# Optimization experiments

Hardware: AMD Instinct MI355X
Metric: run time of the kernel (lower is better)

## Reference

```python
import jax, jax.numpy as jnp
from jax import lax
import numpy as np

EPS = 1e-5
BONES = [(0,1),(0,2),(1,3),(2,4),(5,7),(7,9),(6,8),(8,10),(11,13),(13,15),(12,14),(14,16)]


def _build_adj(num_joints=17):
    adj = np.eye(num_joints, dtype=np.float32)
    for i, j in BONES:
        adj[i, j] = 1.0
        adj[j, i] = 1.0
    d = adj.sum(1) ** -0.5
    return jnp.asarray(d[:, None] * adj * d[None, :])


def _bn(x, gamma, beta, axes):
    # training-mode BatchNorm: biased variance over `axes`
    mean = x.mean(axes, keepdims=True)
    var = ((x - mean) ** 2).mean(axes, keepdims=True)
    return (x - mean) * lax.rsqrt(var + EPS) * gamma + beta


def _gcn_block(x, adj, w, b, gamma, beta):
    # x: [N, V, Cin]; adjacency mixing then 1x1 conv (pointwise linear)
    x = jnp.einsum('nvc,vw->nwc', x, adj)
    x = jnp.einsum('nvc,oc->nvo', x, w) + b            # Conv1d(k=1): [N, V, Cout]
    x = _bn(x, gamma, beta, axes=(0, 1))               # BN over channel Cout
    return jax.nn.relu(x)


def setup_inputs() -> dict:
    key = jax.random.key(0)
    ks = jax.random.split(key, 16)
    B, T, V, C, H = 64, 512, 17, 2, 128
    s = 0.1
    return {
        'x':   jax.random.normal(ks[0], (B, T, V, C), jnp.float32),
        'adj': _build_adj(V),
        'w1':  jax.random.normal(ks[1], (64, C), jnp.float32) * s,
        'b1':  jax.random.normal(ks[2], (64,), jnp.float32) * s,
        'g1':  1.0 + jax.random.normal(ks[3], (64,), jnp.float32) * s,
        'be1': jax.random.normal(ks[4], (64,), jnp.float32) * s,
        'w2':  jax.random.normal(ks[5], (H, 64), jnp.float32) * s,
        'b2':  jax.random.normal(ks[6], (H,), jnp.float32) * s,
        'g2':  1.0 + jax.random.normal(ks[7], (H,), jnp.float32) * s,
        'be2': jax.random.normal(ks[8], (H,), jnp.float32) * s,
        'wt':  jax.random.normal(ks[9], (H, H * V, 3), jnp.float32) * 0.02,
        'bt':  jax.random.normal(ks[10], (H,), jnp.float32) * s,
        'gt':  1.0 + jax.random.normal(ks[11], (H,), jnp.float32) * s,
        'bet': jax.random.normal(ks[12], (H,), jnp.float32) * s,
    }


def reference(x, adj, w1, b1, g1, be1, w2, b2, g2, be2, wt, bt, gt, bet):
    B, T, V, C = x.shape
    h = x.reshape(B * T, V, C)
    h = _gcn_block(h, adj, w1, b1, g1, be1)            # [B*T, V, 64]
    h = _gcn_block(h, adj, w2, b2, g2, be2)            # [B*T, V, H]
    H = h.shape[-1]
    # matches torch: view(B,T,V,H).permute(0,3,1,2).contiguous().view(B,-1,T)
    h = h.reshape(B, T, V, H).transpose(0, 3, 1, 2).reshape(B, H * V, T)
    h = lax.conv_general_dilated(h, wt, (1,), [(1, 1)],
                                 dimension_numbers=('NCH', 'OIH', 'NCH'))
    h = h + bt[None, :, None]                          # [B, H, T]
    h = _bn(h, gt[None, :, None], bet[None, :, None], axes=(0, 2))
    h = jax.nn.relu(h)
    return h.transpose(0, 2, 1)                        # [B, T, H]
```

## Files before the change

kernel.cpp:

```cpp
#include <hip/hip_runtime.h>
#include <hip/hip_bf16.h>

#define EPS 1e-5f

static constexpr int Bv = 64, Tv = 512, Vv = 17, Hv = 128;
static constexpr int CHv = Hv * Vv;
static constexpr long ZBv = (long)CHv * Tv;

typedef __attribute__((ext_vector_type(8))) short short8v;
typedef __attribute__((ext_vector_type(4))) float f32x4;
typedef __attribute__((ext_vector_type(4))) int   int4v;

static constexpr size_t SZ_Z    = (size_t)Bv * (size_t)ZBv * 2;
static constexpr size_t OFF_ZR  = 0;
static constexpr size_t OFF_WKT = OFF_ZR + SZ_Z;
static constexpr size_t SZ_WKT  = (size_t)3 * 128 * 2176 * 2;
static constexpr size_t OFF_W2B = OFF_WKT + SZ_WKT;
static constexpr size_t SZ_W2B  = (size_t)128 * 64 * 2;
static constexpr size_t OFF_CP  = OFF_W2B + SZ_W2B;
static constexpr size_t SZ_CP   = (size_t)Bv * Hv * Tv * 4;
static constexpr size_t OFF_ST  = OFF_CP + SZ_CP;

__device__ __forceinline__ int4v ld16(const __hip_bfloat16* p) {
    return *reinterpret_cast<const int4v*>(p);
}
__device__ __forceinline__ f32x4 mfma16(int4v a, int4v b, f32x4 c) {
    return __builtin_amdgcn_mfma_f32_16x16x32_bf16(
        *reinterpret_cast<short8v*>(&a), *reinterpret_cast<short8v*>(&b), c, 0, 0, 0);
}
__device__ __forceinline__ float bf2f(short s) {
    return __uint_as_float(((unsigned)(unsigned short)s) << 16);
}

__global__ __launch_bounds__(256) void k_wt_bf16(const float* __restrict__ wt,
                                                 __hip_bfloat16* __restrict__ wkt2) {
    int i = blockIdx.x * 256 + threadIdx.x;
    if (i >= 3 * 128 * 2176) return;
    int el = i & 7;
    int ln = (i >> 3) & 63;
    int r  = i >> 9;
    int c  = r % 68; r /= 68;
    int oT = r & 7;  int k = r >> 3;
    int o   = oT * 16 + (ln & 15);
    int cip = c * 32 + ((ln >> 4) << 3) + el;
    int q = cip >> 7, o_in = cip & 127;
    wkt2[i] = __float2bfloat16(wt[(size_t)o * 6528 + (o_in * 17 + q) * 3 + k]);
}

__global__ __launch_bounds__(256) void k_w2b(const float* __restrict__ w2,
                                             __hip_bfloat16* __restrict__ w2b) {
    int e = blockIdx.x * 256 + threadIdx.x;
    if (e >= 8192) return;
    w2b[e] = __float2bfloat16(w2[e]);
}

__global__ __launch_bounds__(256) void k_stats1(const float* __restrict__ x,
                                                const float* __restrict__ adj,
                                                const float* __restrict__ w1,
                                                const float* __restrict__ b1,
                                                float* __restrict__ st) {
    __shared__ float adj_s[289];
    __shared__ float xs[32 * 34];
    __shared__ float mix[32 * 34];
    __shared__ float red[256], red2[256];
    int tid = threadIdx.x;
    int n0 = blockIdx.x * 32;
    for (int i = tid; i < 289; i += 256) adj_s[i] = adj[i];
    for (int i = tid; i < 1088; i += 256) xs[i] = x[(size_t)n0 * 34 + i];
    __syncthreads();
    for (int e = tid; e < 1088; e += 256) {
        int n = e / 34, r = e % 34;
        int w = r >> 1, c = r & 1;
        float acc = 0.f;
        for (int v = 0; v < 17; ++v) acc += xs[n * 34 + v * 2 + c] * adj_s[v * 17 + w];
        mix[n * 34 + w * 2 + c] = acc;
    }
    __syncthreads();
    int o = tid & 63, g = tid >> 6;
    float w0 = w1[o * 2], w1v = w1[o * 2 + 1], bb = b1[o];
    float s = 0.f, s2 = 0.f;
    for (int n = g; n < 32; n += 4)
        for (int v = 0; v < 17; ++v) {
            float a = mix[n * 34 + v * 2] * w0 + mix[n * 34 + v * 2 + 1] * w1v + bb;
            s += a; s2 += a * a;
        }
    red[tid] = s; red2[tid] = s2;
    __syncthreads();
    if (tid < 64) {
        float S  = red[tid] + red[tid + 64] + red[tid + 128] + red[tid + 192];
        float S2 = red2[tid] + red2[tid + 64] + red2[tid + 128] + red2[tid + 192];
        int slot = blockIdx.x & 15;
        atomicAdd(&st[slot * 64 + o], S);
        atomicAdd(&st[1024 + slot * 64 + o], S2);
    }
}

__global__ void k_finalize(const float* __restrict__ sums, const float* __restrict__ sumsq,
                           const float* __restrict__ gamma, const float* __restrict__ beta,
                           float* __restrict__ scale, float* __restrict__ shift,
                           int count, float inv_denom) {
    int o = threadIdx.x;
    if (o >= count) return;
    float S = 0.f, Q = 0.f;
    for (int j = 0; j < 16; ++j) { S += sums[j * count + o]; Q += sumsq[j * count + o]; }
    float m = S * inv_denom;
    float var = Q * inv_denom - m * m;
    float rstd = rsqrtf(var + EPS);
    float sc = rstd * gamma[o];
    scale[o] = sc;
    shift[o] = beta[o] - m * sc;
}

__global__ __launch_bounds__(256) void k_gcn(const float* __restrict__ x,
                                             const float* __restrict__ adj,
                                             const float* __restrict__ w1,
                                             const float* __restrict__ b1,
                                             const float* __restrict__ sc1,
                                             const float* __restrict__ sh1,
                                             const __hip_bfloat16* __restrict__ w2b,
                                             const float* __restrict__ b2,
                                             float* __restrict__ st,
                                             __hip_bfloat16* __restrict__ zr2) {
    __shared__ float adj_s[289];
    __shared__ float xs[170];
    __shared__ float mix1[170];
    __shared__ __align__(16) char uni[26240];
    __hip_bfloat16* h1b  = reinterpret_cast<__hip_bfloat16*>(uni);
    __hip_bfloat16* m2b  = reinterpret_cast<__hip_bfloat16*>(uni + 14976);
    __hip_bfloat16* a2st = reinterpret_cast<__hip_bfloat16*>(uni);

    int tid = threadIdx.x;
    int bi = blockIdx.x;
    int b = bi / 136, rb = bi - b * 136;
    int r0 = rb * 64;
    int t_lo = r0 / 17;

    for (int i = tid; i < 289; i += 256) adj_s[i] = adj[i];
    for (int i = tid; i < 170; i += 256) {
        int tt = i / 34, r = i - tt * 34;
        int t = min(t_lo + tt, 511);
        xs[i] = x[(size_t)(b * 512 + t) * 34 + r];
    }
    __syncthreads();

    for (int e = tid; e < 170; e += 256) {
        int n = e / 34, r = e % 34, w = r >> 1, c = r & 1;
        float acc = 0.f;
        for (int v = 0; v < 17; ++v) acc += xs[n * 34 + v * 2 + c] * adj_s[v * 17 + w];
        mix1[n * 34 + w * 2 + c] = acc;
    }
    __syncthreads();

    for (int e = tid; e < 85 * 64; e += 256) {
        int row = e >> 6, o = e & 63;
        int n = row / 17, v = row - n * 17;
        float a = mix1[n * 34 + v * 2] * w1[o * 2] + mix1[n * 34 + v * 2 + 1] * w1[o * 2 + 1] + b1[o];
        a = a * sc1[o] + sh1[o];
        h1b[row * 88 + o] = __float2bfloat16(fmaxf(a, 0.f));
    }
    __syncthreads();

    {
        int j = tid >> 2, cq = (tid & 3) << 4;
        int tv = r0 + j;
        int t = tv / 17, w = tv - t * 17;
        int base = (t - t_lo) * 17;
        float a[16];
#pragma unroll
        for (int i = 0; i < 16; ++i) a[i] = 0.f;
        for (int v = 0; v < 17; ++v) {
            float ad = adj_s[v * 17 + w];
            short8v p0 = *reinterpret_cast<const short8v*>(&h1b[(base + v) * 88 + cq]);
            short8v p1 = *reinterpret_cast<const short8v*>(&h1b[(base + v) * 88 + cq + 8]);
#pragma unroll
            for (int i = 0; i < 8; ++i) {
                a[i]     += ad * bf2f(p0[i]);
                a[i + 8] += ad * bf2f(p1[i]);
            }
        }
        __hip_bfloat16* mp = &m2b[j * 88 + cq];
#pragma unroll
        for (int i = 0; i < 16; ++i) mp[i] = __float2bfloat16(a[i]);
    }
    __syncthreads();

    int wid = tid >> 6, lane = tid & 63;
    int l15 = lane & 15, l4 = lane >> 4;
    int m0 = (wid >> 1) * 64, nh = (wid & 1) * 32;

    short8v afr[4][2];
#pragma unroll
    for (int mi = 0; mi < 4; ++mi)
#pragma unroll
        for (int kk = 0; kk < 2; ++kk)
            afr[mi][kk] = *reinterpret_cast<const short8v*>(
                w2b + (size_t)(m0 + mi * 16 + l15) * 64 + kk * 32 + l4 * 8);

    f32x4 acc[4][2];
#pragma unroll
    for (int mi = 0; mi < 4; ++mi)
#pragma unroll
        for (int ni = 0; ni < 2; ++ni) acc[mi][ni] = (f32x4){0.f, 0.f, 0.f, 0.f};

#pragma unroll
    for (int kk = 0; kk < 2; ++kk)
#pragma unroll
        for (int ni = 0; ni < 2; ++ni) {
            short8v bfr = *reinterpret_cast<const short8v*>(
                &m2b[(nh + ni * 16 + l15) * 88 + kk * 32 + l4 * 8]);
#pragma unroll
            for (int mi = 0; mi < 4; ++mi)
                acc[mi][ni] = __builtin_amdgcn_mfma_f32_16x16x32_bf16(
                    afr[mi][kk], bfr, acc[mi][ni], 0, 0, 0);
        }
    __syncthreads();

#pragma unroll
    for (int mi = 0; mi < 4; ++mi)
#pragma unroll
        for (int r = 0; r < 4; ++r) {
            int o = m0 + mi * 16 + l4 * 4 + r;
            float bb = b2[o];
            a2st[(nh + l15) * 136 + o]      = __float2bfloat16(acc[mi][0][r] + bb);
            a2st[(nh + 16 + l15) * 136 + o] = __float2bfloat16(acc[mi][1][r] + bb);
        }
    __syncthreads();

    {
        int o = tid & 127, half = tid >> 7;
        float s = 0.f, q = 0.f;
        int j0 = half * 32;
#pragma unroll 8
        for (int j = j0; j < j0 + 32; ++j) {
            float v = bf2f(*reinterpret_cast<const short*>(&a2st[j * 136 + o]));
            s += v; q += v * v;
        }
        int slot = bi & 15;
        atomicAdd(&st[2048 + slot * 128 + o], s);
        atomicAdd(&st[4096 + slot * 128 + o], q);
    }

    int sf0 = r0 & 511;
    int T0 = sf0 >> 4;
    int q  = r0 >> 9;
    for (int e = tid; e < 1024; e += 256) {
        int ft = e >> 6, ln = e & 63;
        int sfti = ft >> 2, cic = ft & 3;
        int row = sfti * 16 + (ln & 15);
        int col = cic * 32 + ((ln >> 4) << 3);
        short8v val = *reinterpret_cast<const short8v*>(&a2st[row * 136 + col]);
        size_t dst = (((size_t)(b * 32 + T0 + sfti) * 68) + (q * 4 + cic)) * 512 + ln * 8;
        *reinterpret_cast<short8v*>(zr2 + dst) = val;
    }
}

__device__ __forceinline__ int4v bnrelu(int4v raw, const float* scr, const float* shr) {
    int4v out;
#pragma unroll
    for (int j = 0; j < 4; ++j) {
        unsigned w = (unsigned)raw[j];
        float lo = __uint_as_float(w << 16);
        float hi = __uint_as_float(w & 0xffff0000u);
        lo = fmaxf(lo * scr[2 * j] + shr[2 * j], 0.f);
        hi = fmaxf(hi * scr[2 * j + 1] + shr[2 * j + 1], 0.f);
        __hip_bfloat162 p = __float22bfloat162_rn(make_float2(lo, hi));
        out[j] = *reinterpret_cast<int*>(&p);
    }
    return out;
}

__global__ __launch_bounds__(256, 2) void k_conv_mfma(const __hip_bfloat16* __restrict__ zr2,
                                                      const __hip_bfloat16* __restrict__ wkt2,
                                                      const float* __restrict__ sc2,
                                                      const float* __restrict__ sh2,
                                                      const float* __restrict__ bt,
                                                      float* __restrict__ cp,
                                                      float* __restrict__ s3,
                                                      float* __restrict__ ss3) {
    __shared__ float scs[128], shs[128];
    __shared__ __align__(16) __hip_bfloat16 zbuf[2][66][40];

    int tid = threadIdx.x;
    if (tid < 128) { scs[tid] = sc2[tid]; shs[tid] = sh2[tid]; }

    int bi = blockIdx.x;
    int b  = bi >> 3;
    int sB = (bi & 7) << 6;
    int T  = sB >> 4;
    int wid = tid >> 6, lane = tid & 63;
    int l15 = lane & 15, l4 = lane >> 4;
    int m0 = (wid >> 1) * 64;
    int n0loc = (wid & 1) * 32;
    int mT = m0 >> 4;

    int sf_f = tid >> 6;
    int srow = sf_f * 16 + l15 + 1;
    int sch  = l4 * 8;
    size_t smain = ((size_t)(b * 32 + T + sf_f) * 68) * 512 + (size_t)lane * 8;
    bool has_edge = tid < 8;
    int er  = tid >> 2;
    int elg = tid & 3;
    int esf = sB - 1 + er * 65;
    bool eok = (unsigned)esf < 512u;
    int erow = er * 65;
    size_t sedge = eok ? (((size_t)(b * 32 + (esf >> 4)) * 68) * 512
                          + (size_t)((elg * 16 + (esf & 15)) * 8)) : 0;

    int aoffE[3][4];
#pragma unroll
    for (int k = 0; k < 3; ++k)
#pragma unroll
        for (int mi = 0; mi < 4; ++mi)
            aoffE[k][mi] = ((k * 8 + mT + mi) * 68) * 512 + lane * 8;

    f32x4 acc[4][2];
#pragma unroll
    for (int mi = 0; mi < 4; ++mi)
#pragma unroll
        for (int ni = 0; ni < 2; ++ni) acc[mi][ni] = (f32x4){0.f, 0.f, 0.f, 0.f};

    __syncthreads();

    {
        int4v mr = ld16(zr2 + smain);
        float scr[8], shr[8];
        *reinterpret_cast<f32x4*>(scr)     = *reinterpret_cast<const f32x4*>(&scs[sch]);
        *reinterpret_cast<f32x4*>(scr + 4) = *reinterpret_cast<const f32x4*>(&scs[sch + 4]);
        *reinterpret_cast<f32x4*>(shr)     = *reinterpret_cast<const f32x4*>(&shs[sch]);
        *reinterpret_cast<f32x4*>(shr + 4) = *reinterpret_cast<const f32x4*>(&shs[sch + 4]);
        *reinterpret_cast<int4v*>(&zbuf[0][srow][sch]) = bnrelu(mr, scr, shr);
        if (has_edge) {
            int4v ev = (int4v){0, 0, 0, 0};
            if (eok) {
                int4v erv = ld16(zr2 + sedge);
                float escr[8], eshr[8];
                int ei = elg * 8;
                *reinterpret_cast<f32x4*>(escr)     = *reinterpret_cast<const f32x4*>(&scs[ei]);
                *reinterpret_cast<f32x4*>(escr + 4) = *reinterpret_cast<const f32x4*>(&scs[ei + 4]);
                *reinterpret_cast<f32x4*>(eshr)     = *reinterpret_cast<const f32x4*>(&shs[ei]);
                *reinterpret_cast<f32x4*>(eshr + 4) = *reinterpret_cast<const f32x4*>(&shs[ei + 4]);
                ev = bnrelu(erv, escr, eshr);
            }
            *reinterpret_cast<int4v*>(&zbuf[0][erow][elg * 8]) = ev;
        }
    }
    __syncthreads();

    int cur = 0;
    for (int c = 0; c < 68; ++c) {
        int c1 = c + 1;
        bool do_stage = c1 < 68;
        int4v mr = (int4v){0, 0, 0, 0}, erv = (int4v){0, 0, 0, 0};
        if (do_stage) {
            mr = ld16(zr2 + smain + ((size_t)c1 << 9));
            if (has_edge && eok) erv = ld16(zr2 + sedge + ((size_t)c1 << 9));
        }
        int4v a_[3][4];
#pragma unroll
        for (int k = 0; k < 3; ++k)
#pragma unroll
            for (int mi = 0; mi < 4; ++mi)
                a_[k][mi] = ld16(wkt2 + (size_t)aoffE[k][mi] + ((size_t)c << 9));
        int4v bf[3][2];
#pragma unroll
        for (int k = 0; k < 3; ++k)
#pragma unroll
            for (int ni = 0; ni < 2; ++ni) {
                int row = n0loc + 1 + ni * 16 + l15 + k - 1;
                bf[k][ni] = *reinterpret_cast<const int4v*>(&zbuf[cur][row][l4 * 8]);
            }
        __builtin_amdgcn_sched_barrier(0);
#pragma unroll
        for (int k = 0; k < 3; ++k)
#pragma unroll
            for (int mi = 0; mi < 4; ++mi)
#pragma unroll
                for (int ni = 0; ni < 2; ++ni)
                    acc[mi][ni] = mfma16(a_[k][mi], bf[k][ni], acc[mi][ni]);
        if (do_stage) {
            int ph = (c1 & 3) << 5;
            float scr[8], shr[8];
            *reinterpret_cast<f32x4*>(scr)     = *reinterpret_cast<const f32x4*>(&scs[ph + sch]);
            *reinterpret_cast<f32x4*>(scr + 4) = *reinterpret_cast<const f32x4*>(&scs[ph + sch + 4]);
            *reinterpret_cast<f32x4*>(shr)     = *reinterpret_cast<const f32x4*>(&shs[ph + sch]);
            *reinterpret_cast<f32x4*>(shr + 4) = *reinterpret_cast<const f32x4*>(&shs[ph + sch + 4]);
            *reinterpret_cast<int4v*>(&zbuf[cur ^ 1][srow][sch]) = bnrelu(mr, scr, shr);
            if (has_edge) {
                int4v ev = (int4v){0, 0, 0, 0};
                if (eok) {
                    int ei = ph + elg * 8;
                    float escr[8], eshr[8];
                    *reinterpret_cast<f32x4*>(escr)     = *reinterpret_cast<const f32x4*>(&scs[ei]);
                    *reinterpret_cast<f32x4*>(escr + 4) = *reinterpret_cast<const f32x4*>(&scs[ei + 4]);
                    *reinterpret_cast<f32x4*>(eshr)     = *reinterpret_cast<const f32x4*>(&shs[ei]);
                    *reinterpret_cast<f32x4*>(eshr + 4) = *reinterpret_cast<const f32x4*>(&shs[ei + 4]);
                    ev = bnrelu(erv, escr, eshr);
                }
                *reinterpret_cast<int4v*>(&zbuf[cur ^ 1][erow][elg * 8]) = ev;
            }
        }
        __syncthreads();
        cur ^= 1;
    }

    int slot = bi & 15;
#pragma unroll
    for (int mi = 0; mi < 4; ++mi)
#pragma unroll
        for (int r = 0; r < 4; ++r) {
            int o = m0 + mi * 16 + l4 * 4 + r;
            float btv = bt[o];
            float v0 = acc[mi][0][r] + btv;
            float v1 = acc[mi][1][r] + btv;
            size_t cb = ((size_t)(b * 128 + o)) * 512 + sB + n0loc + l15;
            cp[cb] = v0;
            cp[cb + 16] = v1;
            float sv = v0 + v1;
            float sq = v0 * v0 + v1 * v1;
#pragma unroll
            for (int off = 1; off < 16; off <<= 1) {
                sv += __shfl_xor(sv, off, 64);
                sq += __shfl_xor(sq, off, 64);
            }
            if (l15 == 0) {
                atomicAdd(&s3[slot * 128 + o], sv);
                atomicAdd(&ss3[slot * 128 + o], sq);
            }
        }
}

__global__ __launch_bounds__(256) void k_out(const float* __restrict__ cp,
                                             const float* __restrict__ sc3,
                                             const float* __restrict__ sh3,
                                             float* __restrict__ out) {
    __shared__ float tile[128 * 33];
    int tid = threadIdx.x;
    int b = blockIdx.x >> 4;
    int t0 = (blockIdx.x & 15) * 32;
    for (int e = tid; e < 128 * 32; e += 256) {
        int o = e >> 5, tj = e & 31;
        tile[o * 33 + tj] = cp[((size_t)b * 128 + o) * 512 + t0 + tj];
    }
    __syncthreads();
    for (int e = tid; e < 128 * 32; e += 256) {
        int o = e & 127, th = e >> 7;
        float v = tile[o * 33 + th] * sc3[o] + sh3[o];
        out[((size_t)b * 512 + t0 + th) * 128 + o] = fmaxf(v, 0.f);
    }
}

extern "C" void kernel_launch(void* const* d_in, const int* in_sizes, int n_in,
                              void* d_out, int out_size, void* d_ws, size_t ws_size,
                              hipStream_t stream) {
    const float* x   = (const float*)d_in[0];
    const float* adj = (const float*)d_in[1];
    const float* w1  = (const float*)d_in[2];
    const float* b1  = (const float*)d_in[3];
    const float* g1  = (const float*)d_in[4];
    const float* be1 = (const float*)d_in[5];
    const float* w2  = (const float*)d_in[6];
    const float* b2  = (const float*)d_in[7];
    const float* g2  = (const float*)d_in[8];
    const float* be2 = (const float*)d_in[9];
    const float* wt  = (const float*)d_in[10];
    const float* bt  = (const float*)d_in[11];
    const float* gt  = (const float*)d_in[12];
    const float* bet = (const float*)d_in[13];
    float* out = (float*)d_out;

    char* ws = (char*)d_ws;
    __hip_bfloat16* zr2  = (__hip_bfloat16*)(ws + OFF_ZR);
    __hip_bfloat16* wkt2 = (__hip_bfloat16*)(ws + OFF_WKT);
    __hip_bfloat16* w2b  = (__hip_bfloat16*)(ws + OFF_W2B);
    float* cp = (float*)(ws + OFF_CP);
    float* st = (float*)(ws + OFF_ST);

    hipMemsetAsync(st, 0, 10240 * sizeof(float), stream);

    k_wt_bf16<<<dim3(3264), dim3(256), 0, stream>>>(wt, wkt2);
    k_w2b<<<dim3(32), dim3(256), 0, stream>>>(w2, w2b);
    k_stats1<<<dim3(1024), dim3(256), 0, stream>>>(x, adj, w1, b1, st);
    k_finalize<<<dim3(1), dim3(128), 0, stream>>>(st, st + 1024, g1, be1,
                                                  st + 10240, st + 10304, 64, 1.f / 557056.f);
    k_gcn<<<dim3(8704), dim3(256), 0, stream>>>(x, adj, w1, b1,
                                                st + 10240, st + 10304,
                                                w2b, b2, st, zr2);
    k_finalize<<<dim3(1), dim3(128), 0, stream>>>(st + 2048, st + 4096, g2, be2,
                                                  st + 10368, st + 10496, 128, 1.f / 557056.f);
    k_conv_mfma<<<dim3(512), dim3(256), 0, stream>>>(zr2, wkt2,
                                                     st + 10368, st + 10496, bt,
                                                     cp, st + 6144, st + 8192);
    k_finalize<<<dim3(1), dim3(128), 0, stream>>>(st + 6144, st + 8192, gt, bet,
                                                  st + 10624, st + 10752, 128, 1.f / 32768.f);
    k_out<<<dim3(1024), dim3(256), 0, stream>>>(cp, st + 10624, st + 10752, out);
}
```

Measured before the change: 202.5 us.

## Compute second adjacency mix with MFMA and fuse BN stats via shuffles

The second graph-adjacency mixing in k_gcn moves from scalar FMA loops to bf16 MFMA. Each block builds a banded selection matrix from adj and stores h1 transposed in shared memory, so the mix becomes a small matrix multiply. The per-channel BatchNorm sum and sum-of-squares are now reduced in registers with cross-lane shuffles, replacing a separate shared-memory pass. This adds more atomics per block (one per wave-column group instead of one per channel-half), and the extra 96-wide K mostly multiplies zeros.

```diff
diff --git a/kernel.cpp b/kernel.cpp
--- a/kernel.cpp
+++ b/kernel.cpp
@@ -124,9 +124,10 @@
     __shared__ float adj_s[289];
     __shared__ float xs[170];
     __shared__ float mix1[170];
-    __shared__ __align__(16) char uni[26240];
-    __hip_bfloat16* h1b  = reinterpret_cast<__hip_bfloat16*>(uni);
-    __hip_bfloat16* m2b  = reinterpret_cast<__hip_bfloat16*>(uni + 14976);
+    __shared__ __align__(16) char uni[26624];
+    __hip_bfloat16* h1t  = reinterpret_cast<__hip_bfloat16*>(uni);
+    __hip_bfloat16* Ssel = reinterpret_cast<__hip_bfloat16*>(uni + 13312);
+    __hip_bfloat16* m2b  = reinterpret_cast<__hip_bfloat16*>(uni + 13312);
     __hip_bfloat16* a2st = reinterpret_cast<__hip_bfloat16*>(uni);
 
     int tid = threadIdx.x;
@@ -135,6 +136,9 @@
     int r0 = rb * 64;
     int t_lo = r0 / 17;
 
+    int wid = tid >> 6, lane = tid & 63;
+    int l15 = lane & 15, l4 = lane >> 4;
+
     for (int i = tid; i < 289; i += 256) adj_s[i] = adj[i];
     for (int i = tid; i < 170; i += 256) {
         int tt = i / 34, r = i - tt * 34;
@@ -149,45 +153,51 @@
         for (int v = 0; v < 17; ++v) acc += xs[n * 34 + v * 2 + c] * adj_s[v * 17 + w];
         mix1[n * 34 + w * 2 + c] = acc;
     }
+    for (int e = tid; e < 1024; e += 256) {
+        int c = e >> 4, k = 80 + (e & 15);
+        h1t[c * 104 + k] = __float2bfloat16(0.f);
+    }
     __syncthreads();
 
     for (int e = tid; e < 85 * 64; e += 256) {
-        int row = e >> 6, o = e & 63;
+        int o = e / 85, row = e - o * 85;
         int n = row / 17, v = row - n * 17;
         float a = mix1[n * 34 + v * 2] * w1[o * 2] + mix1[n * 34 + v * 2 + 1] * w1[o * 2 + 1] + b1[o];
         a = a * sc1[o] + sh1[o];
-        h1b[row * 88 + o] = __float2bfloat16(fmaxf(a, 0.f));
-    }
-    __syncthreads();
-
+        h1t[o * 104 + row] = __float2bfloat16(fmaxf(a, 0.f));
+    }
     {
-        int j = tid >> 2, cq = (tid & 3) << 4;
-        int tv = r0 + j;
-        int t = tv / 17, w = tv - t * 17;
+        int j = tid >> 2, q = tid & 3;
+        int tvg = r0 + j;
+        int t = tvg / 17, w = tvg - t * 17;
         int base = (t - t_lo) * 17;
-        float a[16];
-#pragma unroll
-        for (int i = 0; i < 16; ++i) a[i] = 0.f;
-        for (int v = 0; v < 17; ++v) {
-            float ad = adj_s[v * 17 + w];
-            short8v p0 = *reinterpret_cast<const short8v*>(&h1b[(base + v) * 88 + cq]);
-            short8v p1 = *reinterpret_cast<const short8v*>(&h1b[(base + v) * 88 + cq + 8]);
-#pragma unroll
-            for (int i = 0; i < 8; ++i) {
-                a[i]     += ad * bf2f(p0[i]);
-                a[i + 8] += ad * bf2f(p1[i]);
-            }
-        }
-        __hip_bfloat16* mp = &m2b[j * 88 + cq];
-#pragma unroll
-        for (int i = 0; i < 16; ++i) mp[i] = __float2bfloat16(a[i]);
-    }
-    __syncthreads();
-
-    int wid = tid >> 6, lane = tid & 63;
-    int l15 = lane & 15, l4 = lane >> 4;
+        for (int rr = q * 24; rr < q * 24 + 24; ++rr) {
+            int dv = rr - base;
+            float val = ((unsigned)dv < 17u) ? adj_s[dv * 17 + w] : 0.f;
+            Ssel[j * 104 + rr] = __float2bfloat16(val);
+        }
+    }
+    __syncthreads();
+
+    int mt0 = (wid >> 1) * 2, nt0 = (wid & 1) * 2;
+    f32x4 acc1[2][2];
+#pragma unroll
+    for (int mi = 0; mi < 2; ++mi)
+#pragma unroll
+        for (int ni = 0; ni < 2; ++ni) acc1[mi][ni] = (f32x4){0.f, 0.f, 0.f, 0.f};
+#pragma unroll
+    for (int kk = 0; kk < 3; ++kk) {
+        int ko = kk * 32 + l4 * 8;
+        int4v sa0 = *reinterpret_cast<const int4v*>(&Ssel[(mt0 * 16 + l15) * 104 + ko]);
+        int4v sa1 = *reinterpret_cast<const int4v*>(&Ssel[((mt0 + 1) * 16 + l15) * 104 + ko]);
+        int4v hb0 = *reinterpret_cast<const int4v*>(&h1t[(nt0 * 16 + l15) * 104 + ko]);
+        int4v hb1 = *reinterpret_cast<const int4v*>(&h1t[((nt0 + 1) * 16 + l15) * 104 + ko]);
+        acc1[0][0] = mfma16(sa0, hb0, acc1[0][0]);
+        acc1[0][1] = mfma16(sa0, hb1, acc1[0][1]);
+        acc1[1][0] = mfma16(sa1, hb0, acc1[1][0]);
+        acc1[1][1] = mfma16(sa1, hb1, acc1[1][1]);
+    }
     int m0 = (wid >> 1) * 64, nh = (wid & 1) * 32;
-
     short8v afr[4][2];
 #pragma unroll
     for (int mi = 0; mi < 4; ++mi)
@@ -195,13 +205,25 @@
         for (int kk = 0; kk < 2; ++kk)
             afr[mi][kk] = *reinterpret_cast<const short8v*>(
                 w2b + (size_t)(m0 + mi * 16 + l15) * 64 + kk * 32 + l4 * 8);
+    __syncthreads();
+
+#pragma unroll
+    for (int mi = 0; mi < 2; ++mi)
+#pragma unroll
+        for (int ni = 0; ni < 2; ++ni)
+#pragma unroll
+            for (int r = 0; r < 4; ++r) {
+                int tv = (mt0 + mi) * 16 + l4 * 4 + r;
+                int c  = (nt0 + ni) * 16 + l15;
+                m2b[tv * 88 + c] = __float2bfloat16(acc1[mi][ni][r]);
+            }
+    __syncthreads();
 
     f32x4 acc[4][2];
 #pragma unroll
     for (int mi = 0; mi < 4; ++mi)
 #pragma unroll
         for (int ni = 0; ni < 2; ++ni) acc[mi][ni] = (f32x4){0.f, 0.f, 0.f, 0.f};
-
 #pragma unroll
     for (int kk = 0; kk < 2; ++kk)
 #pragma unroll
@@ -215,30 +237,30 @@
         }
     __syncthreads();
 
+    int slot = bi & 15;
 #pragma unroll
     for (int mi = 0; mi < 4; ++mi)
 #pragma unroll
         for (int r = 0; r < 4; ++r) {
             int o = m0 + mi * 16 + l4 * 4 + r;
             float bb = b2[o];
-            a2st[(nh + l15) * 136 + o]      = __float2bfloat16(acc[mi][0][r] + bb);
-            a2st[(nh + 16 + l15) * 136 + o] = __float2bfloat16(acc[mi][1][r] + bb);
-        }
-    __syncthreads();
-
-    {
-        int o = tid & 127, half = tid >> 7;
-        float s = 0.f, q = 0.f;
-        int j0 = half * 32;
-#pragma unroll 8
-        for (int j = j0; j < j0 + 32; ++j) {
-            float v = bf2f(*reinterpret_cast<const short*>(&a2st[j * 136 + o]));
-            s += v; q += v * v;
-        }
-        int slot = bi & 15;
-        atomicAdd(&st[2048 + slot * 128 + o], s);
-        atomicAdd(&st[4096 + slot * 128 + o], q);
-    }
+            float v0 = acc[mi][0][r] + bb;
+            float v1 = acc[mi][1][r] + bb;
+            a2st[(nh + l15) * 136 + o]      = __float2bfloat16(v0);
+            a2st[(nh + 16 + l15) * 136 + o] = __float2bfloat16(v1);
+            float sv = v0 + v1;
+            float sq = v0 * v0 + v1 * v1;
+#pragma unroll
+            for (int off = 1; off < 16; off <<= 1) {
+                sv += __shfl_xor(sv, off, 64);
+                sq += __shfl_xor(sq, off, 64);
+            }
+            if (l15 == 0) {
+                atomicAdd(&st[2048 + slot * 128 + o], sv);
+                atomicAdd(&st[4096 + slot * 128 + o], sq);
+            }
+        }
+    __syncthreads();
 
     int sf0 = r0 & 511;
     int T0 = sf0 >> 4;
```

Result: slower. 298.7 us (+47.5%).
